# Performance work log

Hardware: AMD Instinct MI355X
Metric: run time of the kernel (lower is better)

## Reference

```python
import jax, jax.numpy as jnp
import numpy as np

N_NODES = 100000
N_EDGES = 1600000
D = 64


def setup_inputs() -> dict:
    key = jax.random.key(0)
    k1, k2, k3, k4 = jax.random.split(key, 4)
    x = jax.random.normal(k1, (N_NODES, D), dtype=jnp.float32)
    edge_index = jax.random.randint(k2, (2, N_EDGES), 0, N_NODES, dtype=jnp.int64)
    edge_attr = jax.random.normal(k3, (N_EDGES, D), dtype=jnp.float32)
    eps = jnp.zeros((1,), dtype=jnp.float32)
    W = jax.random.normal(k4, (D, D), dtype=jnp.float32) * (1.0 / np.sqrt(D))
    b = jnp.zeros((D,), dtype=jnp.float32)
    return {"x": x, "edge_index": edge_index, "edge_attr": edge_attr,
            "eps": eps, "W": W, "b": b}


def reference(x, edge_index, edge_attr, eps, W, b):
    # GIN branch with agg='point', point_encoder='RELU', use_linear=True
    dst, src = edge_index[0], edge_index[1]
    self_element = x * (1.0 + eps[0])                       # [N, D]
    message = jax.nn.relu(x[src] + edge_attr)               # [E, D]
    x_agg = jax.ops.segment_sum(message, dst, num_segments=x.shape[0])  # [N, D]
    h = self_element + x_agg
    return h @ W + b                                        # Linear(d, d_output)
```

## Files before the change

kernel.cpp:

```cpp
#include <hip/hip_runtime.h>

typedef float f4 __attribute__((ext_vector_type(4)));

constexpr int NN = 100000;
constexpr int NE = 1600000;
constexpr int SCAN_BLK = 1024;
constexpr int NB = (NN + SCAN_BLK - 1) / SCAN_BLK;

__device__ __forceinline__ f4 relu_add(f4 a, f4 b) {
    f4 s = a + b;
    s.x = fmaxf(s.x, 0.f);
    s.y = fmaxf(s.y, 0.f);
    s.z = fmaxf(s.z, 0.f);
    s.w = fmaxf(s.w, 0.f);
    return s;
}

__device__ __forceinline__ f4 bf16x4_to_f4(uint2 u) {
    f4 r;
    r.x = __uint_as_float((u.x & 0xFFFFu) << 16);
    r.y = __uint_as_float(u.x & 0xFFFF0000u);
    r.z = __uint_as_float((u.y & 0xFFFFu) << 16);
    r.w = __uint_as_float(u.y & 0xFFFF0000u);
    return r;
}

__device__ __forceinline__ unsigned short f2bf(float f) {
    unsigned u = __float_as_uint(f);
    u = (u + 0x7FFFu + ((u >> 16) & 1u)) >> 16;
    return (unsigned short)u;
}


__global__ __launch_bounds__(256) void k_init(const float* __restrict__ x,
                                              const float* __restrict__ eps,
                                              float* __restrict__ out) {
    const float s = 1.0f + eps[0];
    const float4* x4 = (const float4*)x;
    float4* o4 = (float4*)out;
    const int total = NN * 16;
    for (int i = blockIdx.x * blockDim.x + threadIdx.x; i < total;
         i += gridDim.x * blockDim.x) {
        float4 v = x4[i];
        v.x *= s; v.y *= s; v.z *= s; v.w *= s;
        o4[i] = v;
    }
}

__global__ __launch_bounds__(256) void k_edges(const float* __restrict__ x,
                                               const int* __restrict__ ei,
                                               const float* __restrict__ ea,
                                               float* __restrict__ out) {
    const int* dst = ei;
    const int* src = ei + NE;
    const float4* ea4 = (const float4*)ea;
    const float4* x4 = (const float4*)x;
    const int total = NE * 16;
    for (int g = blockIdx.x * blockDim.x + threadIdx.x; g < total;
         g += gridDim.x * blockDim.x) {
        const int e = g >> 4;
        const int c = g & 15;
        const int s = src[e];
        const int d = dst[e];
        float4 a  = ea4[g];
        float4 xv = x4[s * 16 + c];
        float* base = out + d * 64 + c * 4;
        atomicAdd(base + 0, fmaxf(xv.x + a.x, 0.0f));
        atomicAdd(base + 1, fmaxf(xv.y + a.y, 0.0f));
        atomicAdd(base + 2, fmaxf(xv.z + a.z, 0.0f));
        atomicAdd(base + 3, fmaxf(xv.w + a.w, 0.0f));
    }
}

__global__ __launch_bounds__(256) void k_linear2(const float* __restrict__ W,
                                                 const float* __restrict__ bias,
                                                 float* __restrict__ out) {
    __shared__ float Ws[64 * 64];
    __shared__ float bs[64];
    for (int i = threadIdx.x; i < 1024; i += 256)
        ((float4*)Ws)[i] = ((const float4*)W)[i];
    if (threadIdx.x < 16)
        ((float4*)bs)[threadIdx.x] = ((const float4*)bias)[threadIdx.x];
    __syncthreads();

    const int l16 = threadIdx.x & 15;
    const int gid = (blockIdx.x * 256 + threadIdx.x) >> 4;
    const float4* Ws4 = (const float4*)Ws;
    float4* out4 = (float4*)out;

    const float4 h4 = out4[gid * 16 + l16];
    float4 o = ((const float4*)bs)[l16];
#pragma unroll
    for (int d = 0; d < 64; ++d) {
        const int q = d >> 2;
        const int r = d & 3;
        float hd;
        if (r == 0)      hd = __shfl(h4.x, q, 16);
        else if (r == 1) hd = __shfl(h4.y, q, 16);
        else if (r == 2) hd = __shfl(h4.z, q, 16);
        else             hd = __shfl(h4.w, q, 16);
        const float4 w = Ws4[d * 16 + l16];
        o.x = fmaf(hd, w.x, o.x);
        o.y = fmaf(hd, w.y, o.y);
        o.z = fmaf(hd, w.z, o.z);
        o.w = fmaf(hd, w.w, o.w);
    }
    out4[gid * 16 + l16] = o;
}


__global__ __launch_bounds__(256) void k_cvt_x(const float* __restrict__ x,
                                               unsigned short* __restrict__ xb) {
    const int total = NN * 16;
    const float4* x4 = (const float4*)x;
    for (int i = blockIdx.x * blockDim.x + threadIdx.x; i < total;
         i += gridDim.x * blockDim.x) {
        const float4 v = x4[i];
        ushort4 o;
        o.x = f2bf(v.x); o.y = f2bf(v.y); o.z = f2bf(v.z); o.w = f2bf(v.w);
        ((ushort4*)xb)[i] = o;
    }
}

__global__ __launch_bounds__(256) void k_hist(const int* __restrict__ dst,
                                              int* __restrict__ counts) {
    const int4* d4 = (const int4*)dst;
    const int total = NE / 4;
    for (int i = blockIdx.x * blockDim.x + threadIdx.x; i < total;
         i += gridDim.x * blockDim.x) {
        const int4 d = d4[i];
        atomicAdd(&counts[d.x], 1);
        atomicAdd(&counts[d.y], 1);
        atomicAdd(&counts[d.z], 1);
        atomicAdd(&counts[d.w], 1);
    }
}

__global__ __launch_bounds__(256) void k_scan_block(const int* __restrict__ counts,
                                                    int* __restrict__ offsets,
                                                    int* __restrict__ bsum) {
    __shared__ int sd[256];
    const int t = threadIdx.x;
    const int base = blockIdx.x * SCAN_BLK;
    int c[4];
    int s = 0;
#pragma unroll
    for (int k = 0; k < 4; ++k) {
        const int i = base + t * 4 + k;
        c[k] = (i < NN) ? counts[i] : 0;
        s += c[k];
    }
    sd[t] = s;
    __syncthreads();
#pragma unroll
    for (int off = 1; off < 256; off <<= 1) {
        int v = (t >= off) ? sd[t - off] : 0;
        __syncthreads();
        sd[t] += v;
        __syncthreads();
    }
    int excl = sd[t] - s;
#pragma unroll
    for (int k = 0; k < 4; ++k) {
        const int i = base + t * 4 + k;
        if (i < NN) offsets[i] = excl;
        excl += c[k];
    }
    if (t == 255) bsum[blockIdx.x] = sd[255];
}

__global__ __launch_bounds__(128) void k_scan_sums(const int* __restrict__ bsum,
                                                   int* __restrict__ bsum_ex) {
    __shared__ int sd[128];
    const int t = threadIdx.x;
    const int v = (t < NB) ? bsum[t] : 0;
    sd[t] = v;
    __syncthreads();
#pragma unroll
    for (int off = 1; off < 128; off <<= 1) {
        int u = (t >= off) ? sd[t - off] : 0;
        __syncthreads();
        sd[t] += u;
        __syncthreads();
    }
    bsum_ex[t] = sd[t] - v;
}

__global__ __launch_bounds__(256) void k_scan_add(int* __restrict__ offsets,
                                                  const int* __restrict__ bsum_ex,
                                                  int* __restrict__ cursor) {
    for (int i = blockIdx.x * blockDim.x + threadIdx.x; i < NN;
         i += gridDim.x * blockDim.x) {
        const int v = offsets[i] + bsum_ex[i >> 10];
        offsets[i] = v;
        cursor[i] = v;
    }
    if (blockIdx.x == 0 && threadIdx.x == 0) offsets[NN] = NE;
}

__global__ __launch_bounds__(256) void k_scatter(const int* __restrict__ dst,
                                                 const int* __restrict__ src,
                                                 int* __restrict__ cursor,
                                                 int2* __restrict__ ps) {
    const int4* d4 = (const int4*)dst;
    const int4* s4 = (const int4*)src;
    const int total = NE / 4;
    for (int i = blockIdx.x * blockDim.x + threadIdx.x; i < total;
         i += gridDim.x * blockDim.x) {
        const int4 d = d4[i];
        const int4 s = s4[i];
        const int e = i * 4;
        int p0 = atomicAdd(&cursor[d.x], 1);
        int p1 = atomicAdd(&cursor[d.y], 1);
        int p2 = atomicAdd(&cursor[d.z], 1);
        int p3 = atomicAdd(&cursor[d.w], 1);
        ps[p0] = make_int2(e + 0, s.x);
        ps[p1] = make_int2(e + 1, s.y);
        ps[p2] = make_int2(e + 2, s.z);
        ps[p3] = make_int2(e + 3, s.w);
    }
}

__global__ __launch_bounds__(256, 4) void k_agg_lin(const float* __restrict__ x,
                                                    const unsigned short* __restrict__ xb,
                                                    const float* __restrict__ ea,
                                                    const int* __restrict__ offsets,
                                                    const int2* __restrict__ ps,
                                                    const float* __restrict__ epsp,
                                                    const float* __restrict__ W,
                                                    const float* __restrict__ bias,
                                                    float* __restrict__ out) {
    __shared__ float Ws[64 * 64];
    __shared__ float bs[64];
    for (int i = threadIdx.x; i < 1024; i += 256)
        ((float4*)Ws)[i] = ((const float4*)W)[i];
    if (threadIdx.x < 16)
        ((float4*)bs)[threadIdx.x] = ((const float4*)bias)[threadIdx.x];
    __syncthreads();

    const int l16 = threadIdx.x & 15;
    const int n = (blockIdx.x * 256 + threadIdx.x) >> 4;
    const float epsv = 1.0f + epsp[0];
    const f4* x4 = (const f4*)x;
    const f4* ea4 = (const f4*)ea;
    const f4* Ws4 = (const f4*)Ws;
    f4* out4 = (f4*)out;

    const int beg = offsets[n];
    const int end = offsets[n + 1];
    f4 acc = {0.f, 0.f, 0.f, 0.f};

    int j = beg;
    for (; j + 4 <= end; j += 4) {
        const int2 d0 = ps[j];
        const int2 d1 = ps[j + 1];
        const int2 d2 = ps[j + 2];
        const int2 d3 = ps[j + 3];
        const f4 A0 = ea4[d0.x * 16 + l16];
        const uint2 xu0 = *(const uint2*)&xb[(size_t)d0.y * 64 + l16 * 4];
        const f4 A1 = ea4[d1.x * 16 + l16];
        const uint2 xu1 = *(const uint2*)&xb[(size_t)d1.y * 64 + l16 * 4];
        const f4 A2 = ea4[d2.x * 16 + l16];
        const uint2 xu2 = *(const uint2*)&xb[(size_t)d2.y * 64 + l16 * 4];
        const f4 A3 = ea4[d3.x * 16 + l16];
        const uint2 xu3 = *(const uint2*)&xb[(size_t)d3.y * 64 + l16 * 4];
        acc += relu_add(bf16x4_to_f4(xu0), A0);
        acc += relu_add(bf16x4_to_f4(xu1), A1);
        acc += relu_add(bf16x4_to_f4(xu2), A2);
        acc += relu_add(bf16x4_to_f4(xu3), A3);
    }
    for (; j < end; ++j) {
        const int2 d = ps[j];
        const uint2 xu = *(const uint2*)&xb[(size_t)d.y * 64 + l16 * 4];
        acc += relu_add(bf16x4_to_f4(xu), ea4[d.x * 16 + l16]);
    }

    const f4 xs = x4[n * 16 + l16];
    f4 h;
    h.x = fmaf(xs.x, epsv, acc.x);
    h.y = fmaf(xs.y, epsv, acc.y);
    h.z = fmaf(xs.z, epsv, acc.z);
    h.w = fmaf(xs.w, epsv, acc.w);

    f4 o = ((const f4*)bs)[l16];
#pragma unroll
    for (int d = 0; d < 64; ++d) {
        const int q = d >> 2;
        const int r = d & 3;
        float hd;
        if (r == 0)      hd = __shfl(h.x, q, 16);
        else if (r == 1) hd = __shfl(h.y, q, 16);
        else if (r == 2) hd = __shfl(h.z, q, 16);
        else             hd = __shfl(h.w, q, 16);
        const f4 w = Ws4[d * 16 + l16];
        o.x = fmaf(hd, w.x, o.x);
        o.y = fmaf(hd, w.y, o.y);
        o.z = fmaf(hd, w.z, o.z);
        o.w = fmaf(hd, w.w, o.w);
    }
    out4[n * 16 + l16] = o;
}

extern "C" void kernel_launch(void* const* d_in, const int* in_sizes, int n_in,
                              void* d_out, int out_size, void* d_ws, size_t ws_size,
                              hipStream_t stream) {
    const float* x   = (const float*)d_in[0];
    const int*   ei  = (const int*)d_in[1];
    const float* ea  = (const float*)d_in[2];
    const float* eps = (const float*)d_in[3];
    const float* W   = (const float*)d_in[4];
    const float* b   = (const float*)d_in[5];
    float* out = (float*)d_out;

    const int* dst = ei;
    const int* src = ei + NE;

    int2* ps     = (int2*)d_ws;
    unsigned short* xb = (unsigned short*)(ps + NE);
    int* counts  = (int*)(xb + (size_t)NN * 64);
    int* offsets = counts + NN;
    int* cursor  = offsets + NN + 1;
    int* bsum    = cursor + NN;
    int* bsum_ex = bsum + 128;
    const size_t ws_needed = (size_t)NE * 8 + (size_t)NN * 64 * 2 +
                             (size_t)(3 * NN + 1 + 256) * sizeof(int);

    if (ws_size < ws_needed) {
        k_init<<<2048, 256, 0, stream>>>(x, eps, out);
        k_edges<<<2048, 256, 0, stream>>>(x, ei, ea, out);
        k_linear2<<<NN * 16 / 256, 256, 0, stream>>>(W, b, out);
        return;
    }

    hipMemsetAsync(counts, 0, (size_t)NN * sizeof(int), stream);
    k_cvt_x<<<2048, 256, 0, stream>>>(x, xb);
    k_hist<<<1024, 256, 0, stream>>>(dst, counts);
    k_scan_block<<<NB, 256, 0, stream>>>(counts, offsets, bsum);
    k_scan_sums<<<1, 128, 0, stream>>>(bsum, bsum_ex);
    k_scan_add<<<256, 256, 0, stream>>>(offsets, bsum_ex, cursor);
    k_scatter<<<1024, 256, 0, stream>>>(dst, src, cursor, ps);
    k_agg_lin<<<NN * 16 / 256, 256, 0, stream>>>(x, xb, ea, offsets, ps, eps,
                                                 W, b, out);
}
```

Before: 319.2 us.

## Convert edge_attr to bf16 before aggregation and fuse small preprocessing kernels

Adds a pass inside the scatter kernel that converts edge_attr to bf16, and the aggregation kernel now gathers the bf16 copy. It also fuses the x conversion with the histogram, and merges the block-sum scan with the offset add, to cut kernel launches. The aim is to halve bytes in the random edge_attr gather. The risks are an extra full read and write of the large edge_attr tensor on every call and reduced precision.

```diff
diff --git a/kernel.cpp b/kernel.cpp
--- a/kernel.cpp
+++ b/kernel.cpp
@@ -109,25 +109,25 @@
 }
 
 
-__global__ __launch_bounds__(256) void k_cvt_x(const float* __restrict__ x,
-                                               unsigned short* __restrict__ xb) {
-    const int total = NN * 16;
+__global__ __launch_bounds__(256) void k_cvt_hist(const float* __restrict__ x,
+                                                  const int* __restrict__ dst,
+                                                  unsigned short* __restrict__ xb,
+                                                  int* __restrict__ counts) {
+    const int tid = blockIdx.x * blockDim.x + threadIdx.x;
+    const int nthr = gridDim.x * blockDim.x;
+
     const float4* x4 = (const float4*)x;
-    for (int i = blockIdx.x * blockDim.x + threadIdx.x; i < total;
-         i += gridDim.x * blockDim.x) {
+    const int xtotal = NN * 16;
+    for (int i = tid; i < xtotal; i += nthr) {
         const float4 v = x4[i];
         ushort4 o;
         o.x = f2bf(v.x); o.y = f2bf(v.y); o.z = f2bf(v.z); o.w = f2bf(v.w);
         ((ushort4*)xb)[i] = o;
     }
-}
-
-__global__ __launch_bounds__(256) void k_hist(const int* __restrict__ dst,
-                                              int* __restrict__ counts) {
+
     const int4* d4 = (const int4*)dst;
-    const int total = NE / 4;
-    for (int i = blockIdx.x * blockDim.x + threadIdx.x; i < total;
-         i += gridDim.x * blockDim.x) {
+    const int htotal = NE / 4;
+    for (int i = tid; i < htotal; i += nthr) {
         const int4 d = d4[i];
         atomicAdd(&counts[d.x], 1);
         atomicAdd(&counts[d.y], 1);
@@ -169,44 +169,47 @@
     if (t == 255) bsum[blockIdx.x] = sd[255];
 }
 
-__global__ __launch_bounds__(128) void k_scan_sums(const int* __restrict__ bsum,
-                                                   int* __restrict__ bsum_ex) {
+__global__ __launch_bounds__(256) void k_scan_finish(int* __restrict__ offsets,
+                                                     const int* __restrict__ bsum,
+                                                     int* __restrict__ cursor) {
     __shared__ int sd[128];
     const int t = threadIdx.x;
-    const int v = (t < NB) ? bsum[t] : 0;
-    sd[t] = v;
+    if (t < 128) {
+        const int v = (t < NB) ? bsum[t] : 0;
+        sd[t] = v;
+    }
     __syncthreads();
 #pragma unroll
     for (int off = 1; off < 128; off <<= 1) {
-        int u = (t >= off) ? sd[t - off] : 0;
+        int u = 0;
+        if (t < 128 && t >= off) u = sd[t - off];
         __syncthreads();
-        sd[t] += u;
+        if (t < 128) sd[t] += u;
         __syncthreads();
     }
-    bsum_ex[t] = sd[t] - v;
-}
-
-__global__ __launch_bounds__(256) void k_scan_add(int* __restrict__ offsets,
-                                                  const int* __restrict__ bsum_ex,
-                                                  int* __restrict__ cursor) {
-    for (int i = blockIdx.x * blockDim.x + threadIdx.x; i < NN;
+    for (int i = blockIdx.x * blockDim.x + t; i < NN;
          i += gridDim.x * blockDim.x) {
-        const int v = offsets[i] + bsum_ex[i >> 10];
+        const int b = i >> 10;
+        const int v = offsets[i] + sd[b] - bsum[b];
         offsets[i] = v;
         cursor[i] = v;
     }
-    if (blockIdx.x == 0 && threadIdx.x == 0) offsets[NN] = NE;
-}
-
-__global__ __launch_bounds__(256) void k_scatter(const int* __restrict__ dst,
-                                                 const int* __restrict__ src,
-                                                 int* __restrict__ cursor,
-                                                 int2* __restrict__ ps) {
+    if (blockIdx.x == 0 && t == 0) offsets[NN] = NE;
+}
+
+__global__ __launch_bounds__(256) void k_scatter_cvt(const int* __restrict__ dst,
+                                                     const int* __restrict__ src,
+                                                     int* __restrict__ cursor,
+                                                     int2* __restrict__ ps,
+                                                     const float* __restrict__ ea,
+                                                     unsigned short* __restrict__ eab) {
+    const int tid = blockIdx.x * blockDim.x + threadIdx.x;
+    const int nthr = gridDim.x * blockDim.x;
+
     const int4* d4 = (const int4*)dst;
     const int4* s4 = (const int4*)src;
-    const int total = NE / 4;
-    for (int i = blockIdx.x * blockDim.x + threadIdx.x; i < total;
-         i += gridDim.x * blockDim.x) {
+    const int stotal = NE / 4;
+    for (int i = tid; i < stotal; i += nthr) {
         const int4 d = d4[i];
         const int4 s = s4[i];
         const int e = i * 4;
@@ -219,11 +222,20 @@
         ps[p2] = make_int2(e + 2, s.z);
         ps[p3] = make_int2(e + 3, s.w);
     }
+
+    const float4* ea4 = (const float4*)ea;
+    const int ctotal = NE * 16;
+    for (int i = tid; i < ctotal; i += nthr) {
+        const float4 v = ea4[i];
+        ushort4 o;
+        o.x = f2bf(v.x); o.y = f2bf(v.y); o.z = f2bf(v.z); o.w = f2bf(v.w);
+        ((ushort4*)eab)[i] = o;
+    }
 }
 
 __global__ __launch_bounds__(256, 4) void k_agg_lin(const float* __restrict__ x,
                                                     const unsigned short* __restrict__ xb,
-                                                    const float* __restrict__ ea,
+                                                    const unsigned short* __restrict__ eab,
                                                     const int* __restrict__ offsets,
                                                     const int2* __restrict__ ps,
                                                     const float* __restrict__ epsp,
@@ -242,7 +254,6 @@
     const int n = (blockIdx.x * 256 + threadIdx.x) >> 4;
     const float epsv = 1.0f + epsp[0];
     const f4* x4 = (const f4*)x;
-    const f4* ea4 = (const f4*)ea;
     const f4* Ws4 = (const f4*)Ws;
     f4* out4 = (f4*)out;
 
@@ -256,23 +267,24 @@
         const int2 d1 = ps[j + 1];
         const int2 d2 = ps[j + 2];
         const int2 d3 = ps[j + 3];
-        const f4 A0 = ea4[d0.x * 16 + l16];
+        const uint2 au0 = *(const uint2*)&eab[(size_t)d0.x * 64 + l16 * 4];
         const uint2 xu0 = *(const uint2*)&xb[(size_t)d0.y * 64 + l16 * 4];
-        const f4 A1 = ea4[d1.x * 16 + l16];
+        const uint2 au1 = *(const uint2*)&eab[(size_t)d1.x * 64 + l16 * 4];
         const uint2 xu1 = *(const uint2*)&xb[(size_t)d1.y * 64 + l16 * 4];
-        const f4 A2 = ea4[d2.x * 16 + l16];
+        const uint2 au2 = *(const uint2*)&eab[(size_t)d2.x * 64 + l16 * 4];
         const uint2 xu2 = *(const uint2*)&xb[(size_t)d2.y * 64 + l16 * 4];
-        const f4 A3 = ea4[d3.x * 16 + l16];
+        const uint2 au3 = *(const uint2*)&eab[(size_t)d3.x * 64 + l16 * 4];
         const uint2 xu3 = *(const uint2*)&xb[(size_t)d3.y * 64 + l16 * 4];
-        acc += relu_add(bf16x4_to_f4(xu0), A0);
-        acc += relu_add(bf16x4_to_f4(xu1), A1);
-        acc += relu_add(bf16x4_to_f4(xu2), A2);
-        acc += relu_add(bf16x4_to_f4(xu3), A3);
+        acc += relu_add(bf16x4_to_f4(xu0), bf16x4_to_f4(au0));
+        acc += relu_add(bf16x4_to_f4(xu1), bf16x4_to_f4(au1));
+        acc += relu_add(bf16x4_to_f4(xu2), bf16x4_to_f4(au2));
+        acc += relu_add(bf16x4_to_f4(xu3), bf16x4_to_f4(au3));
     }
     for (; j < end; ++j) {
         const int2 d = ps[j];
+        const uint2 au = *(const uint2*)&eab[(size_t)d.x * 64 + l16 * 4];
         const uint2 xu = *(const uint2*)&xb[(size_t)d.y * 64 + l16 * 4];
-        acc += relu_add(bf16x4_to_f4(xu), ea4[d.x * 16 + l16]);
+        acc += relu_add(bf16x4_to_f4(xu), bf16x4_to_f4(au));
     }
 
     const f4 xs = x4[n * 16 + l16];
@@ -316,14 +328,15 @@
     const int* src = ei + NE;
 
     int2* ps     = (int2*)d_ws;
-    unsigned short* xb = (unsigned short*)(ps + NE);
-    int* counts  = (int*)(xb + (size_t)NN * 64);
+    unsigned short* xb  = (unsigned short*)(ps + NE);
+    unsigned short* eab = xb + (size_t)NN * 64;
+    int* counts  = (int*)(eab + (size_t)NE * 64);
     int* offsets = counts + NN;
     int* cursor  = offsets + NN + 1;
     int* bsum    = cursor + NN;
-    int* bsum_ex = bsum + 128;
-    const size_t ws_needed = (size_t)NE * 8 + (size_t)NN * 64 * 2 +
-                             (size_t)(3 * NN + 1 + 256) * sizeof(int);
+    const size_t ws_needed = (size_t)NE * 8 + (size_t)NN * 128 +
+                             (size_t)NE * 128 +
+                             (size_t)(3 * NN + 1 + 128) * sizeof(int);
 
     if (ws_size < ws_needed) {
         k_init<<<2048, 256, 0, stream>>>(x, eps, out);
@@ -333,12 +346,10 @@
     }
 
     hipMemsetAsync(counts, 0, (size_t)NN * sizeof(int), stream);
-    k_cvt_x<<<2048, 256, 0, stream>>>(x, xb);
-    k_hist<<<1024, 256, 0, stream>>>(dst, counts);
+    k_cvt_hist<<<1024, 256, 0, stream>>>(x, dst, xb, counts);
     k_scan_block<<<NB, 256, 0, stream>>>(counts, offsets, bsum);
-    k_scan_sums<<<1, 128, 0, stream>>>(bsum, bsum_ex);
-    k_scan_add<<<256, 256, 0, stream>>>(offsets, bsum_ex, cursor);
-    k_scatter<<<1024, 256, 0, stream>>>(dst, src, cursor, ps);
-    k_agg_lin<<<NN * 16 / 256, 256, 0, stream>>>(x, xb, ea, offsets, ps, eps,
+    k_scan_finish<<<256, 256, 0, stream>>>(offsets, bsum, cursor);
+    k_scatter_cvt<<<2048, 256, 0, stream>>>(dst, src, cursor, ps, ea, eab);
+    k_agg_lin<<<NN * 16 / 256, 256, 0, stream>>>(x, xb, eab, offsets, ps, eps,
                                                  W, b, out);
 }
```

Result: slower. 390.4 us (+22.3%).
